# Performance work log

Measured on AMD Instinct MI355X. Metric: run time of the kernel, lower is better.

The kernel has to match this reference:

```python
import jax, jax.numpy as jnp
import numpy as np

DIM = 1024
SEQ = 2048
HID = 128
HEADS = 8
DECAY_CONST = SEQ // 512  # 4


def setup_inputs() -> dict:
    key = jax.random.key(0)
    ks = jax.random.split(key, 8)
    x = jax.random.normal(ks[0], (8, DIM, SEQ), dtype=jnp.float32)
    # per-head input projections: Linear(dim, hidden_dim)
    proj_w = jax.random.normal(ks[1], (HEADS, HID, DIM), dtype=jnp.float32) / np.sqrt(DIM)
    proj_b = jax.random.normal(ks[2], (HEADS, HID), dtype=jnp.float32) * 0.01
    # mixer params: weight (seq,), bias (seq,), decay_value scalar per head
    mix_w = jax.random.normal(ks[3], (HEADS, SEQ), dtype=jnp.float32)
    mix_b = jnp.zeros((HEADS, SEQ), dtype=jnp.float32)
    decay_v = jnp.ones((HEADS,), dtype=jnp.float32)
    # output projection Linear(dim, dim)
    out_w = jax.random.normal(ks[4], (DIM, DIM), dtype=jnp.float32) / np.sqrt(DIM)
    out_b = jax.random.normal(ks[5], (DIM,), dtype=jnp.float32) * 0.01
    return {"x": x, "proj_w": proj_w, "proj_b": proj_b, "mix_w": mix_w,
            "mix_b": mix_b, "decay_v": decay_v, "out_w": out_w, "out_b": out_b}


def _decay_matrices(mix_w, decay_v):
    """Build per-head upper-triangular decayed matrices M[h] (S,S).
    First HEADS//2 heads: ColRepeat (value v[j] on column j);
    last HEADS//2 heads: RowRepeat (value v[i] on row i).
    Entry (i,j) for j>=i is v * clip(d,0.9,1)**((j-i)/DECAY_CONST)."""
    S = mix_w.shape[1]
    H2 = HEADS // 2
    i = jnp.arange(S)[:, None]
    j = jnp.arange(S)[None, :]
    mask = j >= i                                  # (S,S)
    expo = jnp.where(mask, (j - i) / DECAY_CONST, 0.0).astype(jnp.float32)
    d = jnp.clip(decay_v, 0.9, 1.0)                # (H,)
    dpow = d[:, None, None] ** expo[None]          # (H,S,S)
    col_v = jnp.broadcast_to(mix_w[:H2, None, :], (H2, S, S))   # v[j]
    row_v = jnp.broadcast_to(mix_w[H2:, :, None], (HEADS - H2, S, S))  # v[i]
    vmat = jnp.concatenate([col_v, row_v], axis=0)  # (H,S,S)
    return jnp.where(mask[None], vmat * dpow, 0.0)


def reference(x, proj_w, proj_b, mix_w, mix_b, decay_v, out_w, out_b):
    # x: (B, E=dim, T=seq)
    x_bte = jnp.transpose(x, (0, 2, 1))                       # (B,T,E)
    proj = jnp.einsum('bte,hde->bhtd', x_bte, proj_w) + proj_b[None, :, None, :]  # (B,H,T,D)
    M = _decay_matrices(mix_w, decay_v)                        # (H,S,S)
    # mixer: out[t'] = sum_t proj[t] * M[t, t'] ; bias is added per-time-step
    mixed = jnp.einsum('bhtd,hts->bhsd', proj, M) + mix_b[None, :, :, None]  # (B,H,S,D)
    B, H, S, D = mixed.shape
    hidden = jnp.transpose(mixed, (0, 2, 1, 3)).reshape(B, S, H * D)  # concat heads
    out = hidden @ out_w.T + out_b                             # (B,S,dim)
    return jnp.transpose(out, (0, 2, 1))                       # (B,dim,S)
```

## Files before the change

### kernel.cpp

```cpp
#include <hip/hip_runtime.h>

#define DIM 1024
#define SEQ 2048
#define HID 128
#define HEADS 8
#define DECAYC 4
#define CHUNK 32
#define NCH (SEQ / CHUNK)
#define BK 64
#define NT (DIM / BK)

typedef __bf16 bf16x8 __attribute__((ext_vector_type(8)));
typedef float f32x4 __attribute__((ext_vector_type(4)));
typedef unsigned short u16x4 __attribute__((ext_vector_type(4)));

__device__ __forceinline__ unsigned short f2bf(float f) {
  union { float f; unsigned u; } v; v.f = f;
  unsigned r = v.u + 0x7fffu + ((v.u >> 16) & 1u);
  return (unsigned short)(r >> 16);
}
__device__ __forceinline__ float bf2f(unsigned short u) {
  union { unsigned u; float f; } v; v.u = ((unsigned)u) << 16;
  return v.f;
}

typedef __attribute__((address_space(1))) const unsigned int* g_u32p;
typedef __attribute__((address_space(3))) unsigned int* l_u32p;

__device__ __forceinline__ void async_ld16(const unsigned short* g, unsigned short* l) {
  __builtin_amdgcn_global_load_lds((g_u32p)g, (l_u32p)l, 16, 0, 0);
}

__global__ void convertk(const float* __restrict__ in, unsigned short* __restrict__ out, int n) {
  int i = blockIdx.x * 256 + threadIdx.x;
  if (i < n) out[i] = f2bf(in[i]);
}

__global__ __launch_bounds__(256) void transpose_x(const float* __restrict__ x,
                                                   unsigned short* __restrict__ xT) {
  __shared__ float tile[64][65];
  const int b = blockIdx.z;
  const int e0 = blockIdx.x * 64;
  const int t0 = blockIdx.y * 64;
  const int tr = threadIdx.x >> 6;
  const int tc = threadIdx.x & 63;
  const float* xp = x + ((size_t)b * DIM + e0) * SEQ + t0;
#pragma unroll
  for (int i = 0; i < 16; ++i) {
    int e = i * 4 + tr;
    tile[e][tc] = xp[(size_t)e * SEQ + tc];
  }
  __syncthreads();
  unsigned short* op = xT + ((size_t)b * SEQ + t0) * DIM + e0;
#pragma unroll
  for (int i = 0; i < 16; ++i) {
    int t = i * 4 + tr;
    op[(size_t)t * DIM + tc] = f2bf(tile[tc][t]);
  }
}

template <int C_BF16, int BIAS_ROW, int MODE>
__global__ __launch_bounds__(512, 2) void gemm256(const unsigned short* __restrict__ A,
                                                  const unsigned short* __restrict__ B,
                                                  void* __restrict__ Cv,
                                                  const float* __restrict__ bias,
                                                  int ldc, long sB, long sC) {
  __shared__ unsigned short lds[65536];

  int m0, n0, z;
  if constexpr (MODE == 1) {
    m0 = (blockIdx.x >> 2) * 256;
    n0 = (blockIdx.x & 3) * 256;
    z = 0;
  } else {
    z = blockIdx.x >> 5;
    m0 = ((blockIdx.x >> 3) & 3) * 256;
    n0 = (blockIdx.x & 7) * 256;
  }
  B += (size_t)sB * z;

  const int tid = threadIdx.x;
  const int lane = tid & 63;
  const int w = tid >> 6;
  const int wm = w >> 2;
  const int wn = w & 3;

  const unsigned short* sp[2][2][2];
#pragma unroll
  for (int j = 0; j < 2; ++j) {
    int c = (w * 2 + j) * 1024 + lane * 16;
    int cs = c ^ (((c >> 7) & 3) << 4);
    int row = cs >> 6;
    int colel = (cs & 63) >> 1;
#pragma unroll
    for (int kh = 0; kh < 2; ++kh) {
      sp[0][kh][j] = A + (size_t)(m0 + row) * DIM + kh * 32 + colel;
      sp[1][kh][j] = B + (size_t)(n0 + row) * DIM + kh * 32 + colel;
    }
  }

  const int r15 = lane & 15;
  const int hi = lane >> 4;
  const int rsw = ((r15 >> 1) & 3) << 4;
  int aoff[8][2], boff[4][2];
#pragma unroll
  for (int fi = 0; fi < 8; ++fi) {
    int byte = ((wm * 128 + fi * 16 + r15) * 64 + hi * 16) ^ rsw;
#pragma unroll
    for (int ks = 0; ks < 2; ++ks) aoff[fi][ks] = ks * 8192 + (byte >> 1);
  }
#pragma unroll
  for (int fj = 0; fj < 4; ++fj) {
    int byte = ((wn * 64 + fj * 16 + r15) * 64 + hi * 16) ^ rsw;
#pragma unroll
    for (int ks = 0; ks < 2; ++ks) boff[fj][ks] = 16384 + ks * 8192 + (byte >> 1);
  }

  f32x4 acc[8][4] = {};

#define STG(dd, op, kh, tgt)                                                    \
  if ((tgt) < NT) {                                                             \
    unsigned short* dst_ = (unsigned short*)lds + (dd) * 32768 + (op) * 16384 + \
                           (kh) * 8192 + w * 1024;                              \
    async_ld16(sp[op][kh][0] + (tgt) * BK, dst_);                               \
    async_ld16(sp[op][kh][1] + (tgt) * BK, dst_ + 512);                         \
  }

#define PHASE(H_, KS_, MIDBAR, STAGE_STMT)                                      \
  {                                                                             \
    bf16x8 af[4], bfr[4];                                                       \
    _Pragma("unroll") for (int i = 0; i < 4; ++i)                               \
        af[i] = *(const bf16x8*)&lb[aoff[(H_) * 4 + i][KS_]];                   \
    _Pragma("unroll") for (int j = 0; j < 4; ++j)                               \
        bfr[j] = *(const bf16x8*)&lb[boff[j][KS_]];                             \
    STAGE_STMT;                                                                 \
    if (MIDBAR) __builtin_amdgcn_s_barrier();                                   \
    asm volatile("s_waitcnt lgkmcnt(0)" ::: "memory");                          \
    __builtin_amdgcn_sched_barrier(0);                                          \
    __builtin_amdgcn_s_setprio(1);                                              \
    _Pragma("unroll") for (int i = 0; i < 4; ++i)                               \
      _Pragma("unroll") for (int j = 0; j < 4; ++j)                             \
        acc[(H_) * 4 + i][j] = __builtin_amdgcn_mfma_f32_16x16x32_bf16(         \
            af[i], bfr[j], acc[(H_) * 4 + i][j], 0, 0, 0);                      \
    __builtin_amdgcn_s_setprio(0);                                              \
    __builtin_amdgcn_s_barrier();                                               \
  }

  STG(0, 0, 0, 0); STG(0, 1, 0, 0); STG(0, 0, 1, 0); STG(0, 1, 1, 0);
  STG(1, 0, 0, 1); STG(1, 1, 0, 1);

#pragma unroll
  for (int t = 0; t < NT; ++t) {
    const int d = t & 1;
    const unsigned short* lb = (const unsigned short*)lds + d * 32768;
    if (t == NT - 1) {
      asm volatile("s_waitcnt vmcnt(0)" ::: "memory");
    } else {
      asm volatile("s_waitcnt vmcnt(4)" ::: "memory");
    }
    __builtin_amdgcn_s_barrier();
    PHASE(0, 0, 0, STG(d ^ 1, 0, 1, t + 1));
    PHASE(1, 0, 1, STG(d ^ 1, 1, 1, t + 1));
    PHASE(0, 1, 1, STG(d, 0, 0, t + 2));
    PHASE(1, 1, 1, STG(d, 1, 0, t + 2));
  }
#undef PHASE
#undef STG

  const int or0 = hi * 4;
#pragma unroll
  for (int fi = 0; fi < 8; ++fi) {
#pragma unroll
    for (int fj = 0; fj < 4; ++fj) {
      const int col = n0 + wn * 64 + fj * 16 + r15;
      const int rowb = m0 + wm * 128 + fi * 16 + or0;
      float cb = BIAS_ROW ? 0.0f : bias[col];
#pragma unroll
      for (int q = 0; q < 4; ++q) {
        const int row = rowb + q;
        float v = acc[fi][fj][q] + (BIAS_ROW ? bias[row] : cb);
        if constexpr (C_BF16) {
          ((unsigned short*)Cv)[(size_t)sC * z + (size_t)row * ldc + col] = f2bf(v);
        } else {
          ((float*)Cv)[(size_t)sC * z + (size_t)row * ldc + col] = v;
        }
      }
    }
  }
}

__global__ __launch_bounds__(256) void scan_carry(const unsigned short* __restrict__ proj,
                                                  float* __restrict__ carry,
                                                  const float* __restrict__ mix_w,
                                                  const float* __restrict__ decay_v) {
  const int b = blockIdx.x >> 6;
  const int c = blockIdx.x & (NCH - 1);
  const int n0 = threadIdx.x * 4;
  const int h = n0 >> 7;
  const float d = fminf(fmaxf(decay_v[h], 0.9f), 1.0f);
  const float r = powf(d, 1.0f / (float)DECAYC);
  const bool colrep = h < (HEADS / 2);
  const u16x4* p = (const u16x4*)(proj + ((size_t)(b * SEQ + c * CHUNK)) * DIM + n0);
  const float* mw = mix_w + h * SEQ + c * CHUNK;
  float s0 = 0.f, s1 = 0.f, s2 = 0.f, s3 = 0.f;
#pragma unroll 8
  for (int t = 0; t < CHUNK; ++t) {
    u16x4 v = p[t * (DIM / 4)];
    float wi = colrep ? 1.0f : mw[t];
    s0 = s0 * r + bf2f(v[0]) * wi;
    s1 = s1 * r + bf2f(v[1]) * wi;
    s2 = s2 * r + bf2f(v[2]) * wi;
    s3 = s3 * r + bf2f(v[3]) * wi;
  }
  f32x4 out = {s0, s1, s2, s3};
  *(f32x4*)(carry + ((size_t)(b * NCH + c)) * DIM + n0) = out;
}

__global__ __launch_bounds__(256) void scan_prefix(float* __restrict__ carry,
                                                   const float* __restrict__ decay_v) {
  const int idx = blockIdx.x * 256 + threadIdx.x;
  const int b = idx >> 10;
  const int n = idx & 1023;
  const int h = n >> 7;
  const float d = fminf(fmaxf(decay_v[h], 0.9f), 1.0f);
  const float r = powf(d, 1.0f / (float)DECAYC);
  const float rL = powf(r, (float)CHUNK);
  float P = 0.0f;
  for (int c = 0; c < NCH; ++c) {
    float* p = carry + ((size_t)(b * NCH + c)) * DIM + n;
    float cc = *p;
    *p = P;
    P = rL * P + cc;
  }
}

__global__ __launch_bounds__(256) void scan_apply(const unsigned short* __restrict__ proj,
                                                  unsigned short* __restrict__ hidden,
                                                  const float* __restrict__ carry,
                                                  const float* __restrict__ mix_w,
                                                  const float* __restrict__ mix_b,
                                                  const float* __restrict__ decay_v) {
  const int b = blockIdx.x >> 6;
  const int c = blockIdx.x & (NCH - 1);
  const int n0 = threadIdx.x * 4;
  const int h = n0 >> 7;
  const float d = fminf(fmaxf(decay_v[h], 0.9f), 1.0f);
  const float r = powf(d, 1.0f / (float)DECAYC);
  const bool colrep = h < (HEADS / 2);
  const size_t base = ((size_t)(b * SEQ + c * CHUNK)) * DIM + n0;
  const u16x4* p = (const u16x4*)(proj + base);
  u16x4* o = (u16x4*)(hidden + base);
  const float* mw = mix_w + h * SEQ + c * CHUNK;
  const float* mb = mix_b + h * SEQ + c * CHUNK;
  f32x4 ci = *(const f32x4*)(carry + ((size_t)(b * NCH + c)) * DIM + n0);
  float s0 = ci[0], s1 = ci[1], s2 = ci[2], s3 = ci[3];
#pragma unroll 8
  for (int t = 0; t < CHUNK; ++t) {
    u16x4 v = p[t * (DIM / 4)];
    float wv = mw[t];
    float wi = colrep ? 1.0f : wv;
    float wo = colrep ? wv : 1.0f;
    float bb = mb[t];
    s0 = s0 * r + bf2f(v[0]) * wi;
    s1 = s1 * r + bf2f(v[1]) * wi;
    s2 = s2 * r + bf2f(v[2]) * wi;
    s3 = s3 * r + bf2f(v[3]) * wi;
    u16x4 ov;
    ov[0] = f2bf(s0 * wo + bb);
    ov[1] = f2bf(s1 * wo + bb);
    ov[2] = f2bf(s2 * wo + bb);
    ov[3] = f2bf(s3 * wo + bb);
    o[t * (DIM / 4)] = ov;
  }
}

extern "C" void kernel_launch(void* const* d_in, const int* in_sizes, int n_in,
                              void* d_out, int out_size, void* d_ws, size_t ws_size,
                              hipStream_t stream) {
  const float* x = (const float*)d_in[0];
  const float* proj_w = (const float*)d_in[1];
  const float* proj_b = (const float*)d_in[2];
  const float* mix_w = (const float*)d_in[3];
  const float* mix_b = (const float*)d_in[4];
  const float* decay_v = (const float*)d_in[5];
  const float* out_w = (const float*)d_in[6];
  const float* out_b = (const float*)d_in[7];

  char* ws = (char*)d_ws;
  unsigned short* xT = (unsigned short*)ws;
  unsigned short* proj = (unsigned short*)(ws + 33554432);
  unsigned short* W1 = (unsigned short*)(ws + 67108864);
  unsigned short* W2 = (unsigned short*)(ws + 69206016);
  unsigned short* hidden = xT;
  float* carryf = (float*)(ws + 67108864);

  const int NW = DIM * DIM;
  convertk<<<dim3((NW + 255) / 256), 256, 0, stream>>>(proj_w, W1, NW);
  convertk<<<dim3((NW + 255) / 256), 256, 0, stream>>>(out_w, W2, NW);
  transpose_x<<<dim3(16, 32, 8), 256, 0, stream>>>(x, xT);

  gemm256<1, 0, 1><<<dim3(256), 512, 0, stream>>>(xT, W1, proj, proj_b, DIM, 0L, 0L);

  scan_carry<<<dim3(8 * NCH), 256, 0, stream>>>(proj, carryf, mix_w, decay_v);
  scan_prefix<<<dim3(8192 / 256), 256, 0, stream>>>(carryf, decay_v);
  scan_apply<<<dim3(8 * NCH), 256, 0, stream>>>(proj, hidden, carryf, mix_w, mix_b, decay_v);

  gemm256<0, 1, 2><<<dim3(256), 512, 0, stream>>>(W2, hidden, d_out, out_b, SEQ,
                                                  (long)SEQ * DIM, (long)DIM * SEQ);
}
```

Before: 129.5 us.

## Fuse x transpose and bf16 conversion into first projection GEMM

Removes the separate transpose_x kernel and lets the first GEMM read fp32 x directly. It converts x to bf16 in registers and writes the transposed, swizzled tile into LDS, while the weight tile still arrives by async global-to-LDS copies. The two weight-conversion kernels are also merged into one launch. This avoids writing and re-reading a 32MB bf16 intermediate and saves launches. In exchange the GEMM main loop does more register work and has higher VGPR pressure, and the strided fp32 loads may stall the pipeline.

Result: slower. 135.4 us (+4.6%).

```diff
diff --git a/kernel.cpp b/kernel.cpp
--- a/kernel.cpp
+++ b/kernel.cpp
@@ -13,6 +13,7 @@
 typedef __bf16 bf16x8 __attribute__((ext_vector_type(8)));
 typedef float f32x4 __attribute__((ext_vector_type(4)));
 typedef unsigned short u16x4 __attribute__((ext_vector_type(4)));
+typedef unsigned short u16x8 __attribute__((ext_vector_type(8)));
 
 __device__ __forceinline__ unsigned short f2bf(float f) {
   union { float f; unsigned u; } v; v.f = f;
@@ -31,31 +32,147 @@
   __builtin_amdgcn_global_load_lds((g_u32p)g, (l_u32p)l, 16, 0, 0);
 }
 
-__global__ void convertk(const float* __restrict__ in, unsigned short* __restrict__ out, int n) {
+__global__ void convertk2(const float* __restrict__ in0, unsigned short* __restrict__ out0,
+                          const float* __restrict__ in1, unsigned short* __restrict__ out1,
+                          int n) {
   int i = blockIdx.x * 256 + threadIdx.x;
-  if (i < n) out[i] = f2bf(in[i]);
-}
-
-__global__ __launch_bounds__(256) void transpose_x(const float* __restrict__ x,
-                                                   unsigned short* __restrict__ xT) {
-  __shared__ float tile[64][65];
-  const int b = blockIdx.z;
-  const int e0 = blockIdx.x * 64;
-  const int t0 = blockIdx.y * 64;
-  const int tr = threadIdx.x >> 6;
-  const int tc = threadIdx.x & 63;
-  const float* xp = x + ((size_t)b * DIM + e0) * SEQ + t0;
-#pragma unroll
-  for (int i = 0; i < 16; ++i) {
-    int e = i * 4 + tr;
-    tile[e][tc] = xp[(size_t)e * SEQ + tc];
-  }
-  __syncthreads();
-  unsigned short* op = xT + ((size_t)b * SEQ + t0) * DIM + e0;
-#pragma unroll
-  for (int i = 0; i < 16; ++i) {
-    int t = i * 4 + tr;
-    op[(size_t)t * DIM + tc] = f2bf(tile[tc][t]);
+  if (i < n) {
+    out0[i] = f2bf(in0[i]);
+    out1[i] = f2bf(in1[i]);
+  }
+}
+
+__global__ __launch_bounds__(512, 2) void gemm1f(const float* __restrict__ x,
+                                                 const unsigned short* __restrict__ W1,
+                                                 unsigned short* __restrict__ proj,
+                                                 const float* __restrict__ bias) {
+  __shared__ unsigned short lds[65536];
+
+  const int m0 = (blockIdx.x >> 2) * 256;
+  const int n0 = (blockIdx.x & 3) * 256;
+  const int b = m0 >> 11;
+  const int t0 = m0 & 2047;
+
+  const int tid = threadIdx.x;
+  const int lane = tid & 63;
+  const int w = tid >> 6;
+  const int wm = w >> 2;
+  const int wn = w & 3;
+
+  const unsigned short* spB[4];
+#pragma unroll
+  for (int j = 0; j < 4; ++j) {
+    int c = j * 8192 + tid * 16;
+    int cs = c ^ (((c >> 9) & 7) << 4);
+    spB[j] = W1 + (size_t)(n0 + (cs >> 7)) * DIM + ((cs & 127) >> 1);
+  }
+
+  const float* xbase = x + ((size_t)b * DIM + w * 8) * SEQ + t0 + lane * 4;
+
+  const int awbyte = (lane * 4) * 128 + ((w * 16) ^ ((lane & 7) << 4));
+
+  const int r15 = lane & 15;
+  const int hi = lane >> 4;
+  int aoff[8][2], boff[4][2];
+#pragma unroll
+  for (int fi = 0; fi < 8; ++fi) {
+    int t = wm * 128 + fi * 16 + r15;
+#pragma unroll
+    for (int ks = 0; ks < 2; ++ks)
+      aoff[fi][ks] = ((t * 128 + ks * 64 + hi * 16) ^ (((t >> 2) & 7) << 4)) >> 1;
+  }
+#pragma unroll
+  for (int fj = 0; fj < 4; ++fj) {
+    int n = wn * 64 + fj * 16 + r15;
+#pragma unroll
+    for (int ks = 0; ks < 2; ++ks)
+      boff[fj][ks] = 16384 + (((n * 128 + ks * 64 + hi * 16) ^ (((n >> 2) & 7) << 4)) >> 1);
+  }
+
+  f32x4 acc[8][4] = {};
+  f32x4 ar[8];
+
+#define ALOAD(tgt)                                                             \
+  _Pragma("unroll") for (int ee = 0; ee < 8; ++ee)                             \
+      ar[ee] = *(const f32x4*)(xbase + ((size_t)(tgt) * BK + ee) * SEQ);
+
+#define BDMA(dd, tgt)                                                          \
+  _Pragma("unroll") for (int j = 0; j < 4; ++j)                                \
+      async_ld16(spB[j] + (size_t)(tgt) * BK,                                  \
+                 (unsigned short*)lds + (dd) * 32768 + 16384 + j * 4096 + tid * 8);
+
+#define AWRITE(dd)                                                             \
+  {                                                                            \
+    char* ab = (char*)lds + (dd) * 65536;                                      \
+    _Pragma("unroll") for (int tt = 0; tt < 4; ++tt) {                         \
+      u16x8 hv;                                                                \
+      _Pragma("unroll") for (int ee = 0; ee < 8; ++ee) hv[ee] = f2bf(ar[ee][tt]); \
+      *(u16x8*)(ab + awbyte + tt * 128) = hv;                                  \
+    }                                                                          \
+  }
+
+  ALOAD(0);
+  BDMA(0, 0);
+  asm volatile("s_waitcnt vmcnt(4)" ::: "memory");
+  AWRITE(0);
+  asm volatile("s_waitcnt vmcnt(0) lgkmcnt(0)" ::: "memory");
+  __builtin_amdgcn_s_barrier();
+
+#pragma unroll
+  for (int t = 0; t < NT; ++t) {
+    const int d = t & 1;
+    const unsigned short* lb = (const unsigned short*)lds + d * 32768;
+    if (t + 1 < NT) {
+      ALOAD(t + 1);
+      BDMA(d ^ 1, t + 1);
+    }
+#pragma unroll
+    for (int ks = 0; ks < 2; ++ks) {
+      bf16x8 bfr[4];
+#pragma unroll
+      for (int j = 0; j < 4; ++j) bfr[j] = *(const bf16x8*)&lb[boff[j][ks]];
+#pragma unroll
+      for (int Hh = 0; Hh < 2; ++Hh) {
+        bf16x8 af[4];
+#pragma unroll
+        for (int i = 0; i < 4; ++i) af[i] = *(const bf16x8*)&lb[aoff[Hh * 4 + i][ks]];
+        asm volatile("s_waitcnt lgkmcnt(0)" ::: "memory");
+        __builtin_amdgcn_sched_barrier(0);
+        __builtin_amdgcn_s_setprio(1);
+#pragma unroll
+        for (int i = 0; i < 4; ++i)
+#pragma unroll
+          for (int j = 0; j < 4; ++j)
+            acc[Hh * 4 + i][j] = __builtin_amdgcn_mfma_f32_16x16x32_bf16(
+                af[i], bfr[j], acc[Hh * 4 + i][j], 0, 0, 0);
+        __builtin_amdgcn_s_setprio(0);
+      }
+    }
+    if (t + 1 < NT) {
+      asm volatile("s_waitcnt vmcnt(4)" ::: "memory");
+      AWRITE(d ^ 1);
+    }
+    asm volatile("s_waitcnt vmcnt(0) lgkmcnt(0)" ::: "memory");
+    __builtin_amdgcn_s_barrier();
+  }
+#undef ALOAD
+#undef BDMA
+#undef AWRITE
+
+  const int or0 = hi * 4;
+#pragma unroll
+  for (int fi = 0; fi < 8; ++fi) {
+#pragma unroll
+    for (int fj = 0; fj < 4; ++fj) {
+      const int col = n0 + wn * 64 + fj * 16 + r15;
+      const int rowb = m0 + wm * 128 + fi * 16 + or0;
+      float cb = bias[col];
+#pragma unroll
+      for (int q = 0; q < 4; ++q) {
+        const int row = rowb + q;
+        proj[(size_t)row * DIM + col] = f2bf(acc[fi][fj][q] + cb);
+      }
+    }
   }
 }
 
@@ -287,19 +404,16 @@
   const float* out_b = (const float*)d_in[7];
 
   char* ws = (char*)d_ws;
-  unsigned short* xT = (unsigned short*)ws;
+  unsigned short* hidden = (unsigned short*)ws;
   unsigned short* proj = (unsigned short*)(ws + 33554432);
   unsigned short* W1 = (unsigned short*)(ws + 67108864);
   unsigned short* W2 = (unsigned short*)(ws + 69206016);
-  unsigned short* hidden = xT;
   float* carryf = (float*)(ws + 67108864);
 
   const int NW = DIM * DIM;
-  convertk<<<dim3((NW + 255) / 256), 256, 0, stream>>>(proj_w, W1, NW);
-  convertk<<<dim3((NW + 255) / 256), 256, 0, stream>>>(out_w, W2, NW);
-  transpose_x<<<dim3(16, 32, 8), 256, 0, stream>>>(x, xT);
-
-  gemm256<1, 0, 1><<<dim3(256), 512, 0, stream>>>(xT, W1, proj, proj_b, DIM, 0L, 0L);
+  convertk2<<<dim3((NW + 255) / 256), 256, 0, stream>>>(proj_w, W1, out_w, W2, NW);
+
+  gemm1f<<<dim3(256), 512, 0, stream>>>(x, W1, proj, proj_b);
 
   scan_carry<<<dim3(8 * NCH), 256, 0, stream>>>(proj, carryf, mix_w, decay_v);
   scan_prefix<<<dim3(8192 / 256), 256, 0, stream>>>(carryf, decay_v);
```

## Fuse prep kernels into one launch and widen scan/transposes to vector accesses

Applied to the files above, without the earlier changes.

Merges the two weight-conversion kernels and the x transpose into a single prep launch, removing two launches. The transpose write now stores 4 bf16 per thread and the weight conversion reads float4, cutting narrow 2-byte stores. The scan kernels process 8 columns per thread with 16-byte loads and stores at 128 threads per block, which halves the thread count and may lower occupancy for these memory-bound kernels.

After: 125.0 us. 1.04x faster.

```diff
diff --git a/kernel.cpp b/kernel.cpp
--- a/kernel.cpp
+++ b/kernel.cpp
@@ -13,6 +13,7 @@
 typedef __bf16 bf16x8 __attribute__((ext_vector_type(8)));
 typedef float f32x4 __attribute__((ext_vector_type(4)));
 typedef unsigned short u16x4 __attribute__((ext_vector_type(4)));
+typedef unsigned short u16x8 __attribute__((ext_vector_type(8)));
 
 __device__ __forceinline__ unsigned short f2bf(float f) {
   union { float f; unsigned u; } v; v.f = f;
@@ -31,31 +32,53 @@
   __builtin_amdgcn_global_load_lds((g_u32p)g, (l_u32p)l, 16, 0, 0);
 }
 
-__global__ void convertk(const float* __restrict__ in, unsigned short* __restrict__ out, int n) {
-  int i = blockIdx.x * 256 + threadIdx.x;
-  if (i < n) out[i] = f2bf(in[i]);
-}
-
-__global__ __launch_bounds__(256) void transpose_x(const float* __restrict__ x,
-                                                   unsigned short* __restrict__ xT) {
-  __shared__ float tile[64][65];
-  const int b = blockIdx.z;
-  const int e0 = blockIdx.x * 64;
-  const int t0 = blockIdx.y * 64;
-  const int tr = threadIdx.x >> 6;
-  const int tc = threadIdx.x & 63;
-  const float* xp = x + ((size_t)b * DIM + e0) * SEQ + t0;
-#pragma unroll
-  for (int i = 0; i < 16; ++i) {
-    int e = i * 4 + tr;
-    tile[e][tc] = xp[(size_t)e * SEQ + tc];
-  }
-  __syncthreads();
-  unsigned short* op = xT + ((size_t)b * SEQ + t0) * DIM + e0;
-#pragma unroll
-  for (int i = 0; i < 16; ++i) {
-    int t = i * 4 + tr;
-    op[(size_t)t * DIM + tc] = f2bf(tile[tc][t]);
+__global__ __launch_bounds__(256) void prep(const float* __restrict__ x,
+                                            unsigned short* __restrict__ xT,
+                                            const float* __restrict__ w1f,
+                                            unsigned short* __restrict__ W1,
+                                            const float* __restrict__ w2f,
+                                            unsigned short* __restrict__ W2) {
+  const int bid = blockIdx.x;
+  if (bid < 4096) {
+    __shared__ float tile[64][65];
+    const int b = bid >> 9;
+    const int rem = bid & 511;
+    const int t0 = (rem >> 4) * 64;
+    const int e0 = (rem & 15) * 64;
+    const int tr = threadIdx.x >> 6;
+    const int tc = threadIdx.x & 63;
+    const float* xp = x + ((size_t)b * DIM + e0) * SEQ + t0;
+#pragma unroll
+    for (int i = 0; i < 16; ++i) {
+      int e = i * 4 + tr;
+      tile[e][tc] = xp[(size_t)e * SEQ + tc];
+    }
+    __syncthreads();
+    unsigned short* op = xT + ((size_t)b * SEQ + t0) * DIM + e0;
+    const int tq = threadIdx.x >> 4;
+    const int e4 = (threadIdx.x & 15) * 4;
+#pragma unroll
+    for (int i = 0; i < 4; ++i) {
+      int t = i * 16 + tq;
+      u16x4 ov;
+      ov[0] = f2bf(tile[e4 + 0][t]);
+      ov[1] = f2bf(tile[e4 + 1][t]);
+      ov[2] = f2bf(tile[e4 + 2][t]);
+      ov[3] = f2bf(tile[e4 + 3][t]);
+      *(u16x4*)&op[(size_t)t * DIM + e4] = ov;
+    }
+  } else {
+    const int wid = bid - 4096;
+    const float* src = (wid < 1024) ? w1f : w2f;
+    unsigned short* dst = (wid < 1024) ? W1 : W2;
+    const int i = (wid & 1023) * 1024 + threadIdx.x * 4;
+    f32x4 v = *(const f32x4*)&src[i];
+    u16x4 ov;
+    ov[0] = f2bf(v[0]);
+    ov[1] = f2bf(v[1]);
+    ov[2] = f2bf(v[2]);
+    ov[3] = f2bf(v[3]);
+    *(u16x4*)&dst[i] = ov;
   }
 }
 
@@ -189,31 +212,30 @@
   }
 }
 
-__global__ __launch_bounds__(256) void scan_carry(const unsigned short* __restrict__ proj,
+__global__ __launch_bounds__(128) void scan_carry(const unsigned short* __restrict__ proj,
                                                   float* __restrict__ carry,
                                                   const float* __restrict__ mix_w,
                                                   const float* __restrict__ decay_v) {
   const int b = blockIdx.x >> 6;
   const int c = blockIdx.x & (NCH - 1);
-  const int n0 = threadIdx.x * 4;
+  const int n0 = threadIdx.x * 8;
   const int h = n0 >> 7;
   const float d = fminf(fmaxf(decay_v[h], 0.9f), 1.0f);
   const float r = powf(d, 1.0f / (float)DECAYC);
   const bool colrep = h < (HEADS / 2);
-  const u16x4* p = (const u16x4*)(proj + ((size_t)(b * SEQ + c * CHUNK)) * DIM + n0);
+  const u16x8* p = (const u16x8*)(proj + ((size_t)(b * SEQ + c * CHUNK)) * DIM + n0);
   const float* mw = mix_w + h * SEQ + c * CHUNK;
-  float s0 = 0.f, s1 = 0.f, s2 = 0.f, s3 = 0.f;
+  float s[8] = {};
 #pragma unroll 8
   for (int t = 0; t < CHUNK; ++t) {
-    u16x4 v = p[t * (DIM / 4)];
+    u16x8 v = p[t * (DIM / 8)];
     float wi = colrep ? 1.0f : mw[t];
-    s0 = s0 * r + bf2f(v[0]) * wi;
-    s1 = s1 * r + bf2f(v[1]) * wi;
-    s2 = s2 * r + bf2f(v[2]) * wi;
-    s3 = s3 * r + bf2f(v[3]) * wi;
-  }
-  f32x4 out = {s0, s1, s2, s3};
-  *(f32x4*)(carry + ((size_t)(b * NCH + c)) * DIM + n0) = out;
+#pragma unroll
+    for (int e = 0; e < 8; ++e) s[e] = s[e] * r + bf2f(v[e]) * wi;
+  }
+  float* cp = carry + ((size_t)(b * NCH + c)) * DIM + n0;
+  *(f32x4*)cp = f32x4{s[0], s[1], s[2], s[3]};
+  *(f32x4*)(cp + 4) = f32x4{s[4], s[5], s[6], s[7]};
 }
 
 __global__ __launch_bounds__(256) void scan_prefix(float* __restrict__ carry,
@@ -234,7 +256,7 @@
   }
 }
 
-__global__ __launch_bounds__(256) void scan_apply(const unsigned short* __restrict__ proj,
+__global__ __launch_bounds__(128) void scan_apply(const unsigned short* __restrict__ proj,
                                                   unsigned short* __restrict__ hidden,
                                                   const float* __restrict__ carry,
                                                   const float* __restrict__ mix_w,
@@ -242,35 +264,38 @@
                                                   const float* __restrict__ decay_v) {
   const int b = blockIdx.x >> 6;
   const int c = blockIdx.x & (NCH - 1);
-  const int n0 = threadIdx.x * 4;
+  const int n0 = threadIdx.x * 8;
   const int h = n0 >> 7;
   const float d = fminf(fmaxf(decay_v[h], 0.9f), 1.0f);
   const float r = powf(d, 1.0f / (float)DECAYC);
   const bool colrep = h < (HEADS / 2);
   const size_t base = ((size_t)(b * SEQ + c * CHUNK)) * DIM + n0;
-  const u16x4* p = (const u16x4*)(proj + base);
-  u16x4* o = (u16x4*)(hidden + base);
+  const u16x8* p = (const u16x8*)(proj + base);
+  u16x8* o = (u16x8*)(hidden + base);
   const float* mw = mix_w + h * SEQ + c * CHUNK;
   const float* mb = mix_b + h * SEQ + c * CHUNK;
-  f32x4 ci = *(const f32x4*)(carry + ((size_t)(b * NCH + c)) * DIM + n0);
-  float s0 = ci[0], s1 = ci[1], s2 = ci[2], s3 = ci[3];
+  const float* cp = carry + ((size_t)(b * NCH + c)) * DIM + n0;
+  float s[8];
+  {
+    f32x4 c0 = *(const f32x4*)cp;
+    f32x4 c1 = *(const f32x4*)(cp + 4);
+#pragma unroll
+    for (int e = 0; e < 4; ++e) { s[e] = c0[e]; s[4 + e] = c1[e]; }
+  }
 #pragma unroll 8
   for (int t = 0; t < CHUNK; ++t) {
-    u16x4 v = p[t * (DIM / 4)];
+    u16x8 v = p[t * (DIM / 8)];
     float wv = mw[t];
     float wi = colrep ? 1.0f : wv;
     float wo = colrep ? wv : 1.0f;
     float bb = mb[t];
-    s0 = s0 * r + bf2f(v[0]) * wi;
-    s1 = s1 * r + bf2f(v[1]) * wi;
-    s2 = s2 * r + bf2f(v[2]) * wi;
-    s3 = s3 * r + bf2f(v[3]) * wi;
-    u16x4 ov;
-    ov[0] = f2bf(s0 * wo + bb);
-    ov[1] = f2bf(s1 * wo + bb);
-    ov[2] = f2bf(s2 * wo + bb);
-    ov[3] = f2bf(s3 * wo + bb);
-    o[t * (DIM / 4)] = ov;
+    u16x8 ov;
+#pragma unroll
+    for (int e = 0; e < 8; ++e) {
+      s[e] = s[e] * r + bf2f(v[e]) * wi;
+      ov[e] = f2bf(s[e] * wo + bb);
+    }
+    o[t * (DIM / 8)] = ov;
   }
 }
 
@@ -294,16 +319,13 @@
   unsigned short* hidden = xT;
   float* carryf = (float*)(ws + 67108864);
 
-  const int NW = DIM * DIM;
-  convertk<<<dim3((NW + 255) / 256), 256, 0, stream>>>(proj_w, W1, NW);
-  convertk<<<dim3((NW + 255) / 256), 256, 0, stream>>>(out_w, W2, NW);
-  transpose_x<<<dim3(16, 32, 8), 256, 0, stream>>>(x, xT);
+  prep<<<dim3(6144), 256, 0, stream>>>(x, xT, proj_w, W1, out_w, W2);
 
   gemm256<1, 0, 1><<<dim3(256), 512, 0, stream>>>(xT, W1, proj, proj_b, DIM, 0L, 0L);
 
-  scan_carry<<<dim3(8 * NCH), 256, 0, stream>>>(proj, carryf, mix_w, decay_v);
+  scan_carry<<<dim3(8 * NCH), 128, 0, stream>>>(proj, carryf, mix_w, decay_v);
   scan_prefix<<<dim3(8192 / 256), 256, 0, stream>>>(carryf, decay_v);
-  scan_apply<<<dim3(8 * NCH), 256, 0, stream>>>(proj, hidden, carryf, mix_w, mix_b, decay_v);
+  scan_apply<<<dim3(8 * NCH), 128, 0, stream>>>(proj, hidden, carryf, mix_w, mix_b, decay_v);
 
   gemm256<0, 1, 2><<<dim3(256), 512, 0, stream>>>(W2, hidden, d_out, out_b, SEQ,
                                                   (long)SEQ * DIM, (long)DIM * SEQ);
```
